# Kernel optimization log

Hardware: AMD Instinct MI355X
Metric: run time of the kernel (lower is better)

Reference implementation:

```python
import jax, jax.numpy as jnp
import numpy as np

H = 16  # number of heads

def setup_inputs() -> dict:
    key = jax.random.key(0)
    ks = jax.random.split(key, 9)
    B, N, D = 2, 2048, 1024
    s = 0.02
    q = jax.random.normal(ks[0], (B, N, D), jnp.float32)
    k = jax.random.normal(ks[1], (B, N, D), jnp.float32)
    v = jax.random.normal(ks[2], (B, N, D), jnp.float32)
    mask = jax.random.randint(ks[3], (B, 1, N, N), 0, 2).astype(bool)
    Wq = jax.random.normal(ks[4], (D, D), jnp.float32) * s
    Wk = jax.random.normal(ks[5], (D, D), jnp.float32) * s
    Wv = jax.random.normal(ks[6], (D, D), jnp.float32) * s
    Wo = jax.random.normal(ks[7], (D, D), jnp.float32) * s
    bq = jnp.zeros((D,), jnp.float32)
    bk = jnp.zeros((D,), jnp.float32)
    bv = jnp.zeros((D,), jnp.float32)
    bo = jnp.zeros((D,), jnp.float32)
    return {"q": q, "k": k, "v": v, "mask": mask,
            "Wq": Wq, "bq": bq, "Wk": Wk, "bk": bk,
            "Wv": Wv, "bv": bv, "Wo": Wo, "bo": bo}


def reference(q, k, v, mask, Wq, bq, Wk, bk, Wv, bv, Wo, bo):
    B, N, D = q.shape
    dk = D // H
    # nn.Linear: x @ W.T + b, then split heads: b n (h d) -> b h n d
    def proj(x, W, b):
        return (x @ W.T + b).reshape(B, N, H, dk).transpose(0, 2, 1, 3)
    qh = proj(q, Wq, bq)  # [B,H,N,dk]
    kh = proj(k, Wk, bk)
    vh = proj(v, Wv, bv)
    # NOTE: original has NO 1/sqrt(dk) scaling
    score = jnp.einsum('bhnd,bhmd->bhnm', qh, kh)
    score = jnp.where(mask, jnp.float32(-1e9), score)
    attn = jax.nn.softmax(score, axis=-1)
    x = jnp.einsum('bhnm,bhmd->bhnd', attn, vh)
    x = x.transpose(0, 2, 1, 3).reshape(B, N, D)  # b h n d -> b n (h d)
    return x @ Wo.T + bo
```

## Files before the change

kernel.cpp:

```cpp
#include <hip/hip_runtime.h>
#include <math.h>

#define BB 2
#define NN 2048
#define DD 1024
#define HH 16
#define DK 64
#define LOG2E 1.4426950408889634f

typedef __attribute__((ext_vector_type(8))) short short8;
typedef __attribute__((ext_vector_type(4))) float f32x4;
typedef __attribute__((ext_vector_type(16))) float f32x16;
typedef __attribute__((ext_vector_type(4))) float f32x4v;
typedef __attribute__((ext_vector_type(8))) unsigned short ushort8;
typedef __attribute__((ext_vector_type(4))) unsigned short ushort4v;
typedef unsigned long long u64;

__device__ __forceinline__ unsigned short f2bf(float f) {
  unsigned u = __float_as_uint(f);
  unsigned r = (u + 0x7FFFu + ((u >> 16) & 1u)) >> 16;
  return (unsigned short)r;
}

__device__ __forceinline__ unsigned cvtpk(float a, float b) {
  unsigned r;
  asm("v_cvt_pk_bf16_f32 %0, %1, %2" : "=v"(r) : "v"(a), "v"(b));
  return r;
}

__device__ __forceinline__ void gload_lds16(const void* g, void* l) {
  auto gp = (const __attribute__((address_space(1))) unsigned int*)(unsigned long long)g;
  auto lp = (__attribute__((address_space(3))) unsigned int*)(unsigned int)(unsigned long long)l;
  __builtin_amdgcn_global_load_lds(gp, lp, 16, 0, 0);
}

__global__ __launch_bounds__(256) void cvt_all(
    const float* __restrict__ q, const float* __restrict__ k, const float* __restrict__ v,
    const float* __restrict__ wq, const float* __restrict__ wk, const float* __restrict__ wv,
    const float* __restrict__ wo, unsigned short* __restrict__ ws)
{
  const long NW = (long)DD * DD;
  const long NX = (long)BB * NN * DD;
  long i = ((long)blockIdx.x * blockDim.x + threadIdx.x) * 8;
  if (i >= 4 * NW + 3 * NX) return;
  const float* src; unsigned short* dst; long off;
  if (i < 4 * NW) {
    int s = (int)(i / NW);
    src = (s == 0) ? wq : (s == 1) ? wk : (s == 2) ? wv : wo;
    off = i - (long)s * NW;
    dst = ws + (long)s * NW + off;
  } else {
    long j = i - 4 * NW;
    int s = (int)(j / NX);
    src = (s == 0) ? q : (s == 1) ? k : v;
    off = j - (long)s * NX;
    dst = ws + 4 * NW + (long)s * NX + off;
  }
  f32x4v a = *(const f32x4v*)(src + off);
  f32x4v b = *(const f32x4v*)(src + off + 4);
  ushort8 o;
  o[0] = f2bf(a[0]); o[1] = f2bf(a[1]); o[2] = f2bf(a[2]); o[3] = f2bf(a[3]);
  o[4] = f2bf(b[0]); o[5] = f2bf(b[1]); o[6] = f2bf(b[2]); o[7] = f2bf(b[3]);
  *(ushort8*)dst = o;
}

__global__ __launch_bounds__(256) void cvt_mask_bits(const void* __restrict__ mask,
                                                     u64* __restrict__ mb, long total64)
{
  const unsigned char* m8 = (const unsigned char*)mask;
  const int l = threadIdx.x & 63;
  unsigned probe = m8[l * 4 + 1] | m8[l * 4 + 2] | m8[l * 4 + 3];
  const bool isBool = (__any(probe != 0) != 0);

  long t = (long)blockIdx.x * blockDim.x + threadIdx.x;
  if (t >= total64) return;
  u64 bits = 0;
  if (isBool) {
    const uint4* p = (const uint4*)(m8 + t * 64);
#pragma unroll
    for (int i = 0; i < 4; ++i) {
      uint4 q4 = p[i];
      unsigned vv[4] = {q4.x, q4.y, q4.z, q4.w};
#pragma unroll
      for (int j = 0; j < 4; ++j)
#pragma unroll
        for (int bb = 0; bb < 4; ++bb)
          bits |= (u64)((vv[j] >> (8 * bb)) & 1u) << (i * 16 + j * 4 + bb);
    }
  } else {
    const int4* p = (const int4*)((const int*)mask + t * 64);
#pragma unroll
    for (int i = 0; i < 16; ++i) {
      int4 q4 = p[i];
      bits |= (u64)(q4.x & 1) << (i * 4);
      bits |= (u64)(q4.y & 1) << (i * 4 + 1);
      bits |= (u64)(q4.z & 1) << (i * 4 + 2);
      bits |= (u64)(q4.w & 1) << (i * 4 + 3);
    }
  }
  const long bb2 = t >> 16;
  const long qq = (t >> 5) & 2047;
  const long tcol = t & 31;
  mb[(bb2 * 32 + tcol) * 2048 + qq] = bits;
}

struct GemmArgs {
  const unsigned short* A;
  const unsigned short* Bw;
  const float* bias;
  void* C;
  int mode;
  float oscale;
};

template<int TM, int BN>
__global__ __launch_bounds__(256) void gemm_bt(GemmArgs ga0, GemmArgs ga1, GemmArgs ga2)
{
  constexpr int K = DD;
  constexpr int Nn = DD;
  constexpr int GX = 1024 / BN;
  constexpr int GY = 4096 / TM;
  constexpr int PERZ = GX * GY;
  constexpr int MF = TM / 32;
  constexpr int NF = BN / 32;
  constexpr int NT = K / 32;
  constexpr int LPS = TM / 64 + BN / 64;
  __shared__ __align__(16) unsigned short As[3][TM * 32];
  __shared__ __align__(16) unsigned short Bs[3][BN * 32];

  int wgid = blockIdx.x + (blockIdx.y + blockIdx.z * GY) * GX;
  const int nwg = (int)gridDim.z * PERZ;
  const int chunk = nwg >> 3;
  wgid = (wgid & 7) * chunk + (wgid >> 3);
  const int zi = wgid / PERZ;
  const int rem = wgid % PERZ;
  const int m0 = (rem / GX) * TM;
  const int n0 = (rem % GX) * BN;
  GemmArgs ga = (zi == 0) ? ga0 : ((zi == 1) ? ga1 : ga2);

  const int tid = threadIdx.x;
  const int lane = tid & 63;
  const int w = tid >> 6;
  const int m_woff = (w >> 1) * (TM / 2);
  const int n_woff = (w & 1) * (BN / 2);
  const int c = lane & 15, g = lane >> 4;

  f32x4 acc[MF][NF];
  const f32x4 z4 = {0.f, 0.f, 0.f, 0.f};
#pragma unroll
  for (int m = 0; m < MF; ++m)
#pragma unroll
    for (int n = 0; n < NF; ++n) acc[m][n] = z4;

  const unsigned short* Ab = ga.A + (long)m0 * K;
  const unsigned short* Bb = ga.Bw + (long)n0 * K;
  const int ar = tid >> 2;
  const int ac = ((tid & 3) ^ (ar & 3)) * 8;

  auto STAGE = [&](int buf, int kk) {
#pragma unroll
    for (int i = 0; i < TM / 64; ++i)
      gload_lds16(Ab + (long)(i * 64 + ar) * K + kk + ac, &As[buf][i * 2048 + tid * 8]);
#pragma unroll
    for (int i = 0; i < BN / 64; ++i)
      gload_lds16(Bb + (long)(i * 64 + ar) * K + kk + ac, &Bs[buf][i * 2048 + tid * 8]);
  };

  STAGE(0, 0);
  STAGE(1, 32);

  const int rswz = (g ^ (c & 3)) * 8;

  for (int t = 0; t < NT; ++t) {
    if (t < NT - 1) {
      if constexpr (LPS == 4)
        asm volatile("s_waitcnt vmcnt(4)" ::: "memory");
      else
        asm volatile("s_waitcnt vmcnt(3)" ::: "memory");
    } else {
      asm volatile("s_waitcnt vmcnt(0)" ::: "memory");
    }
    __builtin_amdgcn_s_barrier();
    __builtin_amdgcn_sched_barrier(0);
    if (t + 2 < NT) STAGE((t + 2) % 3, (t + 2) * 32);

    const int cb = t % 3;
    short8 a[MF], b[NF];
#pragma unroll
    for (int m = 0; m < MF; ++m)
      a[m] = *(const short8*)&As[cb][(m_woff + 16 * m + c) * 32 + rswz];
#pragma unroll
    for (int n = 0; n < NF; ++n)
      b[n] = *(const short8*)&Bs[cb][(n_woff + 16 * n + c) * 32 + rswz];
    __builtin_amdgcn_s_setprio(1);
#pragma unroll
    for (int m = 0; m < MF; ++m)
#pragma unroll
      for (int n = 0; n < NF; ++n)
        acc[m][n] = __builtin_amdgcn_mfma_f32_16x16x32_bf16(a[m], b[n], acc[m][n], 0, 0, 0);
    __builtin_amdgcn_s_setprio(0);
  }

#pragma unroll
  for (int n = 0; n < NF; ++n) {
    const int col = n0 + n_woff + 16 * n + c;
    const float bv = ga.bias[col];
#pragma unroll
    for (int m = 0; m < MF; ++m) {
      const int row0 = m0 + m_woff + 16 * m + 4 * g;
      if (ga.mode == 2) {
        ushort4v pk;
#pragma unroll
        for (int r = 0; r < 4; ++r) pk[r] = f2bf((acc[m][n][r] + bv) * ga.oscale);
        *(ushort4v*)&((unsigned short*)ga.C)[((long)(row0 >> 11) * DD + col) * NN + (row0 & (NN - 1))] = pk;
      } else {
#pragma unroll
        for (int r = 0; r < 4; ++r) {
          const int row = row0 + r;
          const float val = (acc[m][n][r] + bv) * ga.oscale;
          if (ga.mode == 1)
            ((float*)ga.C)[(long)row * Nn + col] = val;
          else
            ((unsigned short*)ga.C)[(long)row * Nn + col] = f2bf(val);
        }
      }
    }
  }
}

__global__ __launch_bounds__(256) void attn_kernel(
    const unsigned short* __restrict__ Q,
    const unsigned short* __restrict__ K,
    const unsigned short* __restrict__ Vt,
    const u64* __restrict__ mb64,
    unsigned short* __restrict__ ctx)
{
  __shared__ __align__(16) unsigned short Ks[3][64 * 64];
  __shared__ __align__(16) unsigned short Vs[3][64 * 64];

  const int tid = threadIdx.x;
  const int lane = tid & 63;
  const int w = tid >> 6;
  const int bid = blockIdx.x;
  const int b = (bid >> 4) & 1, h = bid & 15;
  const int q0 = (bid >> 5) * 128;
  const int l31 = lane & 31;
  const int hi = lane >> 5;
  const int qrow = q0 + 32 * w + l31;

  short8 aq[4];
  {
    const unsigned short* qp = Q + ((long)(b * NN + qrow)) * DD + h * DK + 8 * hi;
    aq[0] = *(const short8*)(qp);
    aq[1] = *(const short8*)(qp + 16);
    aq[2] = *(const short8*)(qp + 32);
    aq[3] = *(const short8*)(qp + 48);
  }

  f32x16 o0, o1, cinit;
#pragma unroll
  for (int r = 0; r < 16; ++r) { o0[r] = 0.f; o1[r] = 0.f; cinit[r] = -28.853901f; }
  float ls0 = 0.f, ls1 = 0.f;

  const unsigned short* Kbase = K + (long)(b * NN) * DD + h * DK;
  const unsigned short* Vbase = Vt + ((long)(b * DD + h * DK)) * NN;
  const u64* mbase = mb64 + (long)(b * 32) * 2048 + qrow;

  const int srow = tid >> 3;
  const int scol = tid & 7;
  const int swcol = scol ^ (srow & 7);

  auto STAGE = [&](int buf, int t) {
#pragma unroll
    for (int hf = 0; hf < 2; ++hf) {
      const int row = srow + 32 * hf;
      gload_lds16(Kbase + (long)(t * 64 + row) * DD + swcol * 8, &Ks[buf][hf * 2048 + tid * 8]);
      gload_lds16(Vbase + (long)row * NN + t * 64 + swcol * 8, &Vs[buf][hf * 2048 + tid * 8]);
    }
  };

  int koffs[8], voff0[4], voff1[4];
#pragma unroll
  for (int sub = 0; sub < 2; ++sub) {
    const int krow = l31 + 32 * sub;
    const int kswz = (l31 & 7) << 3;
#pragma unroll
    for (int i = 0; i < 4; ++i)
      koffs[sub * 4 + i] = krow * 64 + ((16 * i + 8 * hi) ^ kswz);
#pragma unroll
    for (int dblk = 0; dblk < 2; ++dblk) {
      const int vrow = l31 + 32 * dblk;
      voff0[sub * 2 + dblk] = vrow * 64 + ((32 * sub + 8 * hi) ^ kswz);
      voff1[sub * 2 + dblk] = vrow * 64 + ((32 * sub + 16 + 8 * hi) ^ kswz);
    }
  }

  const int sh4 = 4 * hi;

  auto COMPUTE = [&](int cb, unsigned msk0, unsigned msk1) {
    const unsigned short* Kt = &Ks[cb][0];
    const unsigned short* Vtl = &Vs[cb][0];
#pragma unroll
    for (int sub = 0; sub < 2; ++sub) {
      const unsigned m = sub ? msk1 : msk0;

      f32x16 ss = cinit;
      __builtin_amdgcn_s_setprio(1);
#pragma unroll
      for (int i = 0; i < 4; ++i) {
        const short8 kf = *(const short8*)&Kt[koffs[sub * 4 + i]];
        ss = __builtin_amdgcn_mfma_f32_32x32x16_bf16(kf, aq[i], ss, 0, 0, 0);
      }
      __builtin_amdgcn_s_setprio(0);

      unsigned wv[8];
      float lacc = 0.f;
#pragma unroll
      for (int i = 0; i < 8; ++i) {
        const int r0 = 2 * i, r1 = 2 * i + 1;
        const int cr0 = (r0 & 3) + 8 * (r0 >> 2);
        const int cr1 = (r1 & 3) + 8 * (r1 >> 2);
        const float e0 = ((m >> cr0) & 1u) ? -1e9f : ss[r0];
        const float e1 = ((m >> cr1) & 1u) ? -1e9f : ss[r1];
        const float p0 = __builtin_amdgcn_exp2f(e0);
        const float p1 = __builtin_amdgcn_exp2f(e1);
        lacc += p0 + p1;
        wv[i] = cvtpk(p0, p1);
      }
      if (sub == 0) ls0 += lacc; else ls1 += lacc;

      asm("v_permlane32_swap_b32 %0, %1" : "+v"(wv[0]), "+v"(wv[2]));
      asm("v_permlane32_swap_b32 %0, %1" : "+v"(wv[1]), "+v"(wv[3]));
      asm("v_permlane32_swap_b32 %0, %1" : "+v"(wv[4]), "+v"(wv[6]));
      asm("v_permlane32_swap_b32 %0, %1" : "+v"(wv[5]), "+v"(wv[7]));
      union { short8 s; unsigned u[4]; } pa0, pa1;
      pa0.u[0] = wv[0]; pa0.u[1] = wv[1]; pa0.u[2] = wv[2]; pa0.u[3] = wv[3];
      pa1.u[0] = wv[4]; pa1.u[1] = wv[5]; pa1.u[2] = wv[6]; pa1.u[3] = wv[7];

      __builtin_amdgcn_s_setprio(1);
      {
        const short8 vb00 = *(const short8*)&Vtl[voff0[sub * 2 + 0]];
        const short8 vb10 = *(const short8*)&Vtl[voff1[sub * 2 + 0]];
        o0 = __builtin_amdgcn_mfma_f32_32x32x16_bf16(pa0.s, vb00, o0, 0, 0, 0);
        o0 = __builtin_amdgcn_mfma_f32_32x32x16_bf16(pa1.s, vb10, o0, 0, 0, 0);
        const short8 vb01 = *(const short8*)&Vtl[voff0[sub * 2 + 1]];
        const short8 vb11 = *(const short8*)&Vtl[voff1[sub * 2 + 1]];
        o1 = __builtin_amdgcn_mfma_f32_32x32x16_bf16(pa0.s, vb01, o1, 0, 0, 0);
        o1 = __builtin_amdgcn_mfma_f32_32x32x16_bf16(pa1.s, vb11, o1, 0, 0, 0);
      }
      __builtin_amdgcn_s_setprio(0);
    }
  };

  STAGE(0, 0);
  u64 mwA = mbase[0];
  STAGE(1, 1);
  u64 mwB = mbase[2048];

#pragma unroll 1
  for (int t = 0; t < 32; t += 2) {
    asm volatile("s_waitcnt vmcnt(5)" ::: "memory");
    __builtin_amdgcn_s_barrier();
    __builtin_amdgcn_sched_barrier(0);
    {
      const unsigned msk0 = ((unsigned)mwA) >> sh4;
      const unsigned msk1 = ((unsigned)(mwA >> 32)) >> sh4;
      if (t + 2 < 32) {
        STAGE((t + 2) % 3, t + 2);
        mwA = mbase[(long)(t + 2) * 2048];
      }
      COMPUTE(t % 3, msk0, msk1);
    }
    if (t + 1 < 31) asm volatile("s_waitcnt vmcnt(5)" ::: "memory");
    else            asm volatile("s_waitcnt vmcnt(0)" ::: "memory");
    __builtin_amdgcn_s_barrier();
    __builtin_amdgcn_sched_barrier(0);
    {
      const unsigned msk0 = ((unsigned)mwB) >> sh4;
      const unsigned msk1 = ((unsigned)(mwB >> 32)) >> sh4;
      if (t + 3 < 32) {
        STAGE((t + 3) % 3, t + 3);
        mwB = mbase[(long)(t + 3) * 2048];
      }
      COMPUTE((t + 1) % 3, msk0, msk1);
    }
  }

  float lsum = ls0 + ls1;
  lsum += __shfl_xor(lsum, 32);
  const float inv = 1.0f / lsum;

#pragma unroll
  for (int r = 0; r < 16; ++r) {
    const int qr = (r & 3) + 8 * (r >> 2) + 4 * hi;
    const float linv = __shfl(inv, qr);
    const long row = (long)(b * NN + q0 + 32 * w + qr);
    ctx[row * DD + h * DK + l31] = f2bf(o0[r] * linv);
    ctx[row * DD + h * DK + 32 + l31] = f2bf(o1[r] * linv);
  }
}

extern "C" void kernel_launch(void* const* d_in, const int* in_sizes, int n_in,
                              void* d_out, int out_size, void* d_ws, size_t ws_size,
                              hipStream_t stream) {
  const float* q  = (const float*)d_in[0];
  const float* k  = (const float*)d_in[1];
  const float* v  = (const float*)d_in[2];
  const void*  mask = d_in[3];
  const float* Wq = (const float*)d_in[4];
  const float* bq = (const float*)d_in[5];
  const float* Wk = (const float*)d_in[6];
  const float* bk = (const float*)d_in[7];
  const float* Wv = (const float*)d_in[8];
  const float* bv = (const float*)d_in[9];
  const float* Wo = (const float*)d_in[10];
  const float* bo = (const float*)d_in[11];

  unsigned short* ws = (unsigned short*)d_ws;
  const long NW = (long)DD * DD;
  const long NX = (long)BB * NN * DD;
  unsigned short* Wqb = ws;
  unsigned short* Wkb = ws + NW;
  unsigned short* Wvb = ws + 2 * NW;
  unsigned short* Wob = ws + 3 * NW;
  unsigned short* Xq  = ws + 4 * NW;
  unsigned short* Xk  = Xq + NX;
  unsigned short* Xv  = Xk + NX;
  unsigned short* Qh  = Xv + NX;
  unsigned short* Kh  = Qh + NX;
  unsigned short* Vtr = Kh + NX;
  unsigned short* Ctx = Vtr + NX;
  u64* Mbits = (u64*)(Ctx + NX);
  const long NM64 = (long)BB * NN * NN / 64;

  cvt_all<<<8192, 256, 0, stream>>>(q, k, v, Wq, Wk, Wv, Wo, ws);
  cvt_mask_bits<<<(int)(NM64 / 256), 256, 0, stream>>>(mask, Mbits, NM64);

  GemmArgs gq = {Xq, Wqb, bq, (void*)Qh, 0, LOG2E};
  GemmArgs gk = {Xk, Wkb, bk, (void*)Kh, 0, 1.0f};
  GemmArgs gv = {Xv, Wvb, bv, (void*)Vtr, 2, 1.0f};
  dim3 gproj(DD / 128, (BB * NN) / 128, 3);
  gemm_bt<128, 128><<<gproj, 256, 0, stream>>>(gq, gk, gv);

  attn_kernel<<<512, 256, 0, stream>>>(Qh, Kh, Vtr, Mbits, Ctx);

  GemmArgs go = {Ctx, Wob, bo, d_out, 1, 1.0f};
  dim3 gout(DD / 128, (BB * NN) / 64, 1);
  gemm_bt<64, 128><<<gout, 256, 0, stream>>>(go, go, go);
}
```

Before: 136.4 us.

## Load attention K/V fragments directly into registers and fuse conversion kernels

The attention kernel drops its triple-buffered LDS staging and the barriers around it. Each wave now loads its K and V MFMA fragments straight from global memory into registers, double-buffering K across tiles and overlapping the loads with compute. This removes LDS traffic and block synchronisation, but the four waves in a block each fetch the same K/V tiles, which raises L2/global traffic and register pressure. Separately, the bf16 conversion and mask bit-packing kernels are merged into one launch to save a kernel launch.

New measurement: 201.7 us. +47.8%, slower.

```diff
diff --git a/kernel.cpp b/kernel.cpp
--- a/kernel.cpp
+++ b/kernel.cpp
@@ -34,74 +34,74 @@
   __builtin_amdgcn_global_load_lds(gp, lp, 16, 0, 0);
 }
 
-__global__ __launch_bounds__(256) void cvt_all(
+__global__ __launch_bounds__(256) void cvt_fused(
     const float* __restrict__ q, const float* __restrict__ k, const float* __restrict__ v,
     const float* __restrict__ wq, const float* __restrict__ wk, const float* __restrict__ wv,
-    const float* __restrict__ wo, unsigned short* __restrict__ ws)
+    const float* __restrict__ wo, const void* __restrict__ mask,
+    unsigned short* __restrict__ ws, u64* __restrict__ mb)
 {
-  const long NW = (long)DD * DD;
-  const long NX = (long)BB * NN * DD;
-  long i = ((long)blockIdx.x * blockDim.x + threadIdx.x) * 8;
-  if (i >= 4 * NW + 3 * NX) return;
-  const float* src; unsigned short* dst; long off;
-  if (i < 4 * NW) {
-    int s = (int)(i / NW);
-    src = (s == 0) ? wq : (s == 1) ? wk : (s == 2) ? wv : wo;
-    off = i - (long)s * NW;
-    dst = ws + (long)s * NW + off;
+  if (blockIdx.x < 8192) {
+    const long NW = (long)DD * DD;
+    const long NX = (long)BB * NN * DD;
+    long i = ((long)blockIdx.x * blockDim.x + threadIdx.x) * 8;
+    if (i >= 4 * NW + 3 * NX) return;
+    const float* src; unsigned short* dst; long off;
+    if (i < 4 * NW) {
+      int s = (int)(i / NW);
+      src = (s == 0) ? wq : (s == 1) ? wk : (s == 2) ? wv : wo;
+      off = i - (long)s * NW;
+      dst = ws + (long)s * NW + off;
+    } else {
+      long j = i - 4 * NW;
+      int s = (int)(j / NX);
+      src = (s == 0) ? q : (s == 1) ? k : v;
+      off = j - (long)s * NX;
+      dst = ws + 4 * NW + (long)s * NX + off;
+    }
+    f32x4v a = *(const f32x4v*)(src + off);
+    f32x4v b2 = *(const f32x4v*)(src + off + 4);
+    ushort8 o;
+    o[0] = f2bf(a[0]); o[1] = f2bf(a[1]); o[2] = f2bf(a[2]); o[3] = f2bf(a[3]);
+    o[4] = f2bf(b2[0]); o[5] = f2bf(b2[1]); o[6] = f2bf(b2[2]); o[7] = f2bf(b2[3]);
+    *(ushort8*)dst = o;
   } else {
-    long j = i - 4 * NW;
-    int s = (int)(j / NX);
-    src = (s == 0) ? q : (s == 1) ? k : v;
-    off = j - (long)s * NX;
-    dst = ws + 4 * NW + (long)s * NX + off;
-  }
-  f32x4v a = *(const f32x4v*)(src + off);
-  f32x4v b = *(const f32x4v*)(src + off + 4);
-  ushort8 o;
-  o[0] = f2bf(a[0]); o[1] = f2bf(a[1]); o[2] = f2bf(a[2]); o[3] = f2bf(a[3]);
-  o[4] = f2bf(b[0]); o[5] = f2bf(b[1]); o[6] = f2bf(b[2]); o[7] = f2bf(b[3]);
-  *(ushort8*)dst = o;
-}
-
-__global__ __launch_bounds__(256) void cvt_mask_bits(const void* __restrict__ mask,
-                                                     u64* __restrict__ mb, long total64)
-{
-  const unsigned char* m8 = (const unsigned char*)mask;
-  const int l = threadIdx.x & 63;
-  unsigned probe = m8[l * 4 + 1] | m8[l * 4 + 2] | m8[l * 4 + 3];
-  const bool isBool = (__any(probe != 0) != 0);
-
-  long t = (long)blockIdx.x * blockDim.x + threadIdx.x;
-  if (t >= total64) return;
-  u64 bits = 0;
-  if (isBool) {
-    const uint4* p = (const uint4*)(m8 + t * 64);
-#pragma unroll
-    for (int i = 0; i < 4; ++i) {
-      uint4 q4 = p[i];
-      unsigned vv[4] = {q4.x, q4.y, q4.z, q4.w};
-#pragma unroll
-      for (int j = 0; j < 4; ++j)
-#pragma unroll
-        for (int bb = 0; bb < 4; ++bb)
-          bits |= (u64)((vv[j] >> (8 * bb)) & 1u) << (i * 16 + j * 4 + bb);
-    }
-  } else {
-    const int4* p = (const int4*)((const int*)mask + t * 64);
-#pragma unroll
-    for (int i = 0; i < 16; ++i) {
-      int4 q4 = p[i];
-      bits |= (u64)(q4.x & 1) << (i * 4);
-      bits |= (u64)(q4.y & 1) << (i * 4 + 1);
-      bits |= (u64)(q4.z & 1) << (i * 4 + 2);
-      bits |= (u64)(q4.w & 1) << (i * 4 + 3);
-    }
-  }
-  const long bb2 = t >> 16;
-  const long qq = (t >> 5) & 2047;
-  const long tcol = t & 31;
-  mb[(bb2 * 32 + tcol) * 2048 + qq] = bits;
+    const long total64 = (long)BB * NN * NN / 64;
+    const unsigned char* m8 = (const unsigned char*)mask;
+    const int l = threadIdx.x & 63;
+    unsigned probe = m8[l * 4 + 1] | m8[l * 4 + 2] | m8[l * 4 + 3];
+    const bool isBool = (__any(probe != 0) != 0);
+
+    long t = (long)(blockIdx.x - 8192) * blockDim.x + threadIdx.x;
+    if (t >= total64) return;
+    u64 bits = 0;
+    if (isBool) {
+      const uint4* p = (const uint4*)(m8 + t * 64);
+#pragma unroll
+      for (int i = 0; i < 4; ++i) {
+        uint4 q4 = p[i];
+        unsigned vv[4] = {q4.x, q4.y, q4.z, q4.w};
+#pragma unroll
+        for (int j = 0; j < 4; ++j)
+#pragma unroll
+          for (int bb = 0; bb < 4; ++bb)
+            bits |= (u64)((vv[j] >> (8 * bb)) & 1u) << (i * 16 + j * 4 + bb);
+      }
+    } else {
+      const int4* p = (const int4*)((const int*)mask + t * 64);
+#pragma unroll
+      for (int i = 0; i < 16; ++i) {
+        int4 q4 = p[i];
+        bits |= (u64)(q4.x & 1) << (i * 4);
+        bits |= (u64)(q4.y & 1) << (i * 4 + 1);
+        bits |= (u64)(q4.z & 1) << (i * 4 + 2);
+        bits |= (u64)(q4.w & 1) << (i * 4 + 3);
+      }
+    }
+    const long bb2 = t >> 16;
+    const long qq = (t >> 5) & 2047;
+    const long tcol = t & 31;
+    mb[(bb2 * 32 + tcol) * 2048 + qq] = bits;
+  }
 }
 
 struct GemmArgs {
@@ -235,9 +235,6 @@
     const u64* __restrict__ mb64,
     unsigned short* __restrict__ ctx)
 {
-  __shared__ __align__(16) unsigned short Ks[3][64 * 64];
-  __shared__ __align__(16) unsigned short Vs[3][64 * 64];
-
   const int tid = threadIdx.x;
   const int lane = tid & 63;
   const int w = tid >> 6;
@@ -262,44 +259,38 @@
   for (int r = 0; r < 16; ++r) { o0[r] = 0.f; o1[r] = 0.f; cinit[r] = -28.853901f; }
   float ls0 = 0.f, ls1 = 0.f;
 
-  const unsigned short* Kbase = K + (long)(b * NN) * DD + h * DK;
-  const unsigned short* Vbase = Vt + ((long)(b * DD + h * DK)) * NN;
+  const unsigned short* Kr0 = K + ((long)(b * NN) + l31) * DD + h * DK + 8 * hi;
+  const unsigned short* Kr1 = Kr0 + 32 * DD;
+  const unsigned short* V0 = Vt + ((long)(b * DD + h * DK) + l31) * NN + 8 * hi;
+  const unsigned short* V1 = V0 + 32 * NN;
   const u64* mbase = mb64 + (long)(b * 32) * 2048 + qrow;
 
-  const int srow = tid >> 3;
-  const int scol = tid & 7;
-  const int swcol = scol ^ (srow & 7);
-
-  auto STAGE = [&](int buf, int t) {
-#pragma unroll
-    for (int hf = 0; hf < 2; ++hf) {
-      const int row = srow + 32 * hf;
-      gload_lds16(Kbase + (long)(t * 64 + row) * DD + swcol * 8, &Ks[buf][hf * 2048 + tid * 8]);
-      gload_lds16(Vbase + (long)row * NN + t * 64 + swcol * 8, &Vs[buf][hf * 2048 + tid * 8]);
+  short8 kbA[8], kbB[8], vf[8];
+
+  auto LOADK = [&](int t, short8 (&kb)[8]) {
+    const long toff = (long)t * 64 * DD;
+#pragma unroll
+    for (int i = 0; i < 4; ++i) {
+      kb[i]     = *(const short8*)(Kr0 + toff + 16 * i);
+      kb[4 + i] = *(const short8*)(Kr1 + toff + 16 * i);
     }
   };
-
-  int koffs[8], voff0[4], voff1[4];
-#pragma unroll
-  for (int sub = 0; sub < 2; ++sub) {
-    const int krow = l31 + 32 * sub;
-    const int kswz = (l31 & 7) << 3;
-#pragma unroll
-    for (int i = 0; i < 4; ++i)
-      koffs[sub * 4 + i] = krow * 64 + ((16 * i + 8 * hi) ^ kswz);
-#pragma unroll
-    for (int dblk = 0; dblk < 2; ++dblk) {
-      const int vrow = l31 + 32 * dblk;
-      voff0[sub * 2 + dblk] = vrow * 64 + ((32 * sub + 8 * hi) ^ kswz);
-      voff1[sub * 2 + dblk] = vrow * 64 + ((32 * sub + 16 + 8 * hi) ^ kswz);
-    }
-  }
+  auto LOADV = [&](int t) {
+#pragma unroll
+    for (int sub = 0; sub < 2; ++sub)
+#pragma unroll
+      for (int ks = 0; ks < 2; ++ks) {
+        const int off = t * 64 + 32 * sub + 16 * ks;
+        vf[sub * 4 + ks * 2 + 0] = *(const short8*)(V0 + off);
+        vf[sub * 4 + ks * 2 + 1] = *(const short8*)(V1 + off);
+      }
+  };
 
   const int sh4 = 4 * hi;
 
-  auto COMPUTE = [&](int cb, unsigned msk0, unsigned msk1) {
-    const unsigned short* Kt = &Ks[cb][0];
-    const unsigned short* Vtl = &Vs[cb][0];
+  auto COMPUTE = [&](const short8 (&kb)[8], u64 mword) {
+    const unsigned msk0 = ((unsigned)mword) >> sh4;
+    const unsigned msk1 = ((unsigned)(mword >> 32)) >> sh4;
 #pragma unroll
     for (int sub = 0; sub < 2; ++sub) {
       const unsigned m = sub ? msk1 : msk0;
@@ -307,10 +298,8 @@
       f32x16 ss = cinit;
       __builtin_amdgcn_s_setprio(1);
 #pragma unroll
-      for (int i = 0; i < 4; ++i) {
-        const short8 kf = *(const short8*)&Kt[koffs[sub * 4 + i]];
-        ss = __builtin_amdgcn_mfma_f32_32x32x16_bf16(kf, aq[i], ss, 0, 0, 0);
-      }
+      for (int i = 0; i < 4; ++i)
+        ss = __builtin_amdgcn_mfma_f32_32x32x16_bf16(kb[sub * 4 + i], aq[i], ss, 0, 0, 0);
       __builtin_amdgcn_s_setprio(0);
 
       unsigned wv[8];
@@ -338,52 +327,29 @@
       pa1.u[0] = wv[4]; pa1.u[1] = wv[5]; pa1.u[2] = wv[6]; pa1.u[3] = wv[7];
 
       __builtin_amdgcn_s_setprio(1);
-      {
-        const short8 vb00 = *(const short8*)&Vtl[voff0[sub * 2 + 0]];
-        const short8 vb10 = *(const short8*)&Vtl[voff1[sub * 2 + 0]];
-        o0 = __builtin_amdgcn_mfma_f32_32x32x16_bf16(pa0.s, vb00, o0, 0, 0, 0);
-        o0 = __builtin_amdgcn_mfma_f32_32x32x16_bf16(pa1.s, vb10, o0, 0, 0, 0);
-        const short8 vb01 = *(const short8*)&Vtl[voff0[sub * 2 + 1]];
-        const short8 vb11 = *(const short8*)&Vtl[voff1[sub * 2 + 1]];
-        o1 = __builtin_amdgcn_mfma_f32_32x32x16_bf16(pa0.s, vb01, o1, 0, 0, 0);
-        o1 = __builtin_amdgcn_mfma_f32_32x32x16_bf16(pa1.s, vb11, o1, 0, 0, 0);
-      }
+      o0 = __builtin_amdgcn_mfma_f32_32x32x16_bf16(pa0.s, vf[sub * 4 + 0], o0, 0, 0, 0);
+      o0 = __builtin_amdgcn_mfma_f32_32x32x16_bf16(pa1.s, vf[sub * 4 + 2], o0, 0, 0, 0);
+      o1 = __builtin_amdgcn_mfma_f32_32x32x16_bf16(pa0.s, vf[sub * 4 + 1], o1, 0, 0, 0);
+      o1 = __builtin_amdgcn_mfma_f32_32x32x16_bf16(pa1.s, vf[sub * 4 + 3], o1, 0, 0, 0);
       __builtin_amdgcn_s_setprio(0);
     }
   };
 
-  STAGE(0, 0);
-  u64 mwA = mbase[0];
-  STAGE(1, 1);
-  u64 mwB = mbase[2048];
+  LOADK(0, kbA);
+  u64 mwA = mbase[0], mwB;
 
 #pragma unroll 1
   for (int t = 0; t < 32; t += 2) {
-    asm volatile("s_waitcnt vmcnt(5)" ::: "memory");
-    __builtin_amdgcn_s_barrier();
-    __builtin_amdgcn_sched_barrier(0);
-    {
-      const unsigned msk0 = ((unsigned)mwA) >> sh4;
-      const unsigned msk1 = ((unsigned)(mwA >> 32)) >> sh4;
-      if (t + 2 < 32) {
-        STAGE((t + 2) % 3, t + 2);
-        mwA = mbase[(long)(t + 2) * 2048];
-      }
-      COMPUTE(t % 3, msk0, msk1);
-    }
-    if (t + 1 < 31) asm volatile("s_waitcnt vmcnt(5)" ::: "memory");
-    else            asm volatile("s_waitcnt vmcnt(0)" ::: "memory");
-    __builtin_amdgcn_s_barrier();
-    __builtin_amdgcn_sched_barrier(0);
-    {
-      const unsigned msk0 = ((unsigned)mwB) >> sh4;
-      const unsigned msk1 = ((unsigned)(mwB >> 32)) >> sh4;
-      if (t + 3 < 32) {
-        STAGE((t + 3) % 3, t + 3);
-        mwB = mbase[(long)(t + 3) * 2048];
-      }
-      COMPUTE((t + 1) % 3, msk0, msk1);
-    }
+    LOADV(t);
+    LOADK(t + 1, kbB);
+    mwB = mbase[(long)(t + 1) * 2048];
+    COMPUTE(kbA, mwA);
+    LOADV(t + 1);
+    if (t + 2 < 32) {
+      LOADK(t + 2, kbA);
+      mwA = mbase[(long)(t + 2) * 2048];
+    }
+    COMPUTE(kbB, mwB);
   }
 
   float lsum = ls0 + ls1;
@@ -431,10 +397,8 @@
   unsigned short* Vtr = Kh + NX;
   unsigned short* Ctx = Vtr + NX;
   u64* Mbits = (u64*)(Ctx + NX);
-  const long NM64 = (long)BB * NN * NN / 64;
-
-  cvt_all<<<8192, 256, 0, stream>>>(q, k, v, Wq, Wk, Wv, Wo, ws);
-  cvt_mask_bits<<<(int)(NM64 / 256), 256, 0, stream>>>(mask, Mbits, NM64);
+
+  cvt_fused<<<8704, 256, 0, stream>>>(q, k, v, Wq, Wk, Wv, Wo, mask, ws, Mbits);
 
   GemmArgs gq = {Xq, Wqb, bq, (void*)Qh, 0, LOG2E};
   GemmArgs gk = {Xk, Wkb, bk, (void*)Kh, 0, 1.0f};
```
